# Optimization experiments

Measured on AMD Instinct MI355X. Metric: run time of the kernel, lower is better.

## Reference

```python
import jax, jax.numpy as jnp
import numpy as np

B, S, DIM = 2, 2048, 4096
N_HEADS, N_KV_HEADS = 32, 8
HEAD_DIM = DIM // N_HEADS  # 128
N_REP = N_HEADS // N_KV_HEADS  # 4
NEG_INF = -1e9


def setup_inputs() -> dict:
    key = jax.random.key(0)
    ks = jax.random.split(key, 6)
    x = jax.random.normal(ks[0], (B, S, DIM), dtype=jnp.float32)
    # torch Linear weights are [out_features, in_features]
    sc = 0.02
    wq = jax.random.normal(ks[1], (N_HEADS * HEAD_DIM, DIM), dtype=jnp.float32) * sc
    wk = jax.random.normal(ks[2], (N_KV_HEADS * HEAD_DIM, DIM), dtype=jnp.float32) * sc
    wv = jax.random.normal(ks[3], (N_KV_HEADS * HEAD_DIM, DIM), dtype=jnp.float32) * sc
    wo = jax.random.normal(ks[4], (DIM, N_HEADS * HEAD_DIM), dtype=jnp.float32) * sc
    # RoPE frequencies, matching llama precompute_freqs_cis (theta=10000)
    inv = 1.0 / (10000.0 ** (np.arange(0, HEAD_DIM, 2, dtype=np.float32) / HEAD_DIM))
    t = np.arange(S, dtype=np.float32)
    freqs = np.outer(t, inv)  # [S, HEAD_DIM//2]
    freqs_cos = jnp.asarray(np.cos(freqs), dtype=jnp.float32)
    freqs_sin = jnp.asarray(np.sin(freqs), dtype=jnp.float32)
    # causal mask: 0 on/below diagonal, large negative above
    mask = jnp.triu(jnp.full((S, S), NEG_INF, dtype=jnp.float32), k=1)
    return {"x": x, "wq": wq, "wk": wk, "wv": wv, "wo": wo,
            "freqs_cos": freqs_cos, "freqs_sin": freqs_sin,
            "mask": mask, "start_pos": 0}


def _apply_rope(t, cos, sin):
    # t: [b, s, h, hd]; complex mult on interleaved (even, odd) pairs
    tr, ti = t[..., 0::2], t[..., 1::2]
    cos = cos[None, :, None, :]
    sin = sin[None, :, None, :]
    out_r = tr * cos - ti * sin
    out_i = tr * sin + ti * cos
    return jnp.stack([out_r, out_i], axis=-1).reshape(t.shape)


def reference(x, wq, wk, wv, wo, freqs_cos, freqs_sin, mask, start_pos):
    bsz, seqlen, _ = x.shape
    xq = (x @ wq.T).reshape(bsz, seqlen, N_HEADS, HEAD_DIM)
    xk = (x @ wk.T).reshape(bsz, seqlen, N_KV_HEADS, HEAD_DIM)
    xv = (x @ wv.T).reshape(bsz, seqlen, N_KV_HEADS, HEAD_DIM)
    xq = _apply_rope(xq, freqs_cos, freqs_sin)
    xk = _apply_rope(xk, freqs_cos, freqs_sin)
    # prefill: start_pos == 0, so cache slice == current keys/values
    # GQA repeat_kv via broadcast (torch repeat_interleave over head dim)
    keys = jnp.broadcast_to(xk[:, :, :, None, :],
                            (bsz, seqlen, N_KV_HEADS, N_REP, HEAD_DIM)
                            ).reshape(bsz, seqlen, N_HEADS, HEAD_DIM)
    values = jnp.broadcast_to(xv[:, :, :, None, :],
                              (bsz, seqlen, N_KV_HEADS, N_REP, HEAD_DIM)
                              ).reshape(bsz, seqlen, N_HEADS, HEAD_DIM)
    scale = 1.0 / jnp.sqrt(jnp.float32(HEAD_DIM))
    # [b, h, q, k]
    scores = jnp.einsum('bqhd,bkhd->bhqk', xq, keys) * scale
    scores = scores + mask[None, None, :, :]
    probs = jax.nn.softmax(scores.astype(jnp.float32), axis=-1).astype(xq.dtype)
    out = jnp.einsum('bhqk,bkhd->bqhd', probs, values)
    out = out.reshape(bsz, seqlen, N_HEADS * HEAD_DIM)
    return out @ wo.T
```

## Files before the change

### kernel.cpp

```cpp
#include <hip/hip_runtime.h>

typedef unsigned short u16;
typedef unsigned int u32;
typedef __bf16 bf16_t;
typedef bf16_t bf16x8 __attribute__((ext_vector_type(8)));
typedef float f32x4 __attribute__((ext_vector_type(4)));

#define B_ 2
#define S_ 2048
#define DIM_ 4096
#define NH_ 32
#define NKV_ 8
#define HD_ 128

__device__ __forceinline__ u16 f2b(float f) {
  union { float f; unsigned u; } x; x.f = f;
  unsigned r = x.u + 0x7fffu + ((x.u >> 16) & 1u);
  return (u16)(r >> 16);
}
__device__ __forceinline__ float b2f(u16 u) {
  union { unsigned u; float f; } x; x.u = ((unsigned)u) << 16;
  return x.f;
}
__device__ __forceinline__ u32 cvtpk(float lo, float hi) {
  u32 r;
  asm volatile("v_cvt_pk_bf16_f32 %0, %1, %2" : "=v"(r) : "v"(lo), "v"(hi));
  return r;
}

#define GLDS(gsrc, ldst) \
  __builtin_amdgcn_global_load_lds((const __attribute__((address_space(1))) void*)(gsrc), \
                                   (__attribute__((address_space(3))) void*)(ldst), 16, 0, 0)
#define BAR()    __builtin_amdgcn_s_barrier()
#define SCHED0() __builtin_amdgcn_sched_barrier(0)

__global__ void cvt_kernel(const float* __restrict__ in, u16* __restrict__ out, int n4) {
  int i = blockIdx.x * blockDim.x + threadIdx.x;
  int stride = gridDim.x * blockDim.x;
  for (; i < n4; i += stride) {
    float4 v = ((const float4*)in)[i];
    ushort4 o;
    o.x = f2b(v.x); o.y = f2b(v.y); o.z = f2b(v.z); o.w = f2b(v.w);
    ((ushort4*)out)[i] = o;
  }
}

__global__ void rope_kernel(u16* __restrict__ t, const float* __restrict__ fc,
                            const float* __restrict__ fs, int nheads) {
  int idx = blockIdx.x * blockDim.x + threadIdx.x;
  int ppr = nheads * 64;
  int row = idx / ppr;
  int pr = idx - row * ppr;
  int h = pr >> 6, j = pr & 63;
  int s = row & (S_ - 1);
  float c = fc[s * 64 + j], sn = fs[s * 64 + j];
  u16* p = t + (size_t)row * (size_t)(nheads * HD_) + h * HD_ + j * 2;
  float tr = b2f(p[0]), ti = b2f(p[1]);
  p[0] = f2b(tr * c - ti * sn);
  p[1] = f2b(tr * sn + ti * c);
}

template<int MODE>
__global__ __launch_bounds__(512, 2) void gemm256(const u16* __restrict__ A,
                                                  const u16* __restrict__ B,
                                                  void* __restrict__ Cout,
                                                  void* __restrict__ Cout2,
                                                  int M, int N, int K) {
  __shared__ u16 As[2][2][128 * 64];
  __shared__ u16 Bs[2][2][128 * 64];
  const int nbn = N >> 8;
  const int nwg = gridDim.x;
  int wg = blockIdx.x;
  wg = (wg & 7) * (nwg >> 3) + (wg >> 3);
  const int bm = wg / nbn;
  const int bn = wg - bm * nbn;
  const int tid = threadIdx.x;
  const int lane = tid & 63;
  const int wv = tid >> 6;
  const int wm = wv >> 2, wn = wv & 3;
  const int qloc = lane & 15, grp = lane >> 4;
  const int NT = K >> 6;

  f32x4 acc[8][4];
#pragma unroll
  for (int i = 0; i < 8; i++)
#pragma unroll
    for (int j = 0; j < 4; j++)
#pragma unroll
      for (int r = 0; r < 4; r++) acc[i][j][r] = 0.0f;

  const int srowl = lane >> 3;
  const int scsw = 8 * ((lane & 7) ^ srowl);
  const size_t rowA = (size_t)(bm * 256 + wv * 16 + srowl) * K + scsw;
  const size_t rowB = (size_t)(bn * 256 + wv * 16 + srowl) * K + scsw;

#define STAGE_A(buf, h, tt) { \
    GLDS(A + rowA + (size_t)((h) * 128) * K + (size_t)(tt) * 64, &As[buf][h][wv * 1024]); \
    GLDS(A + rowA + (size_t)((h) * 128 + 8) * K + (size_t)(tt) * 64, &As[buf][h][wv * 1024 + 512]); }
#define STAGE_B(buf, h, tt) { \
    GLDS(B + rowB + (size_t)((h) * 128) * K + (size_t)(tt) * 64, &Bs[buf][h][wv * 1024]); \
    GLDS(B + rowB + (size_t)((h) * 128 + 8) * K + (size_t)(tt) * 64, &Bs[buf][h][wv * 1024 + 512]); }

  STAGE_A(0, 0, 0); STAGE_A(0, 1, 0);
  STAGE_B(0, 0, 0); STAGE_B(0, 1, 0);
  STAGE_B(1, 0, 1); STAGE_B(1, 1, 1);
  asm volatile("s_waitcnt vmcnt(4)" ::: "memory");
  BAR();

  for (int t = 0; t < NT; t += 2) {
#pragma unroll
    for (int half = 0; half < 2; half++) {
      bf16x8 bfr[4][2];
#pragma unroll
      for (int qd = 0; qd < 4; qd++) {
        if (qd == 0) {
#pragma unroll
          for (int j = 0; j < 4; j++)
#pragma unroll
            for (int ks = 0; ks < 2; ks++) {
              int rb = (wn & 1) * 64 + j * 16 + qloc;
              bfr[j][ks] = *(const bf16x8*)((const char*)&Bs[half][wn >> 1][0]
                           + rb * 128 + ((ks * 64 + grp * 16) ^ ((rb & 7) << 4)));
            }
        }
        bf16x8 af[2][2];
#pragma unroll
        for (int ii = 0; ii < 2; ii++)
#pragma unroll
          for (int ks = 0; ks < 2; ks++) {
            int rh = qd * 32 + ii * 16 + qloc;
            af[ii][ks] = *(const bf16x8*)((const char*)&As[half][wm][0]
                         + rh * 128 + ((ks * 64 + grp * 16) ^ ((rh & 7) << 4)));
          }
        const int ph = half * 4 + qd;
        if (ph == 0)      { STAGE_A(1, 0, t + 1); }
        else if (ph == 1) { STAGE_A(1, 1, t + 1); }
        else if (ph == 2) { if (t + 2 < NT) STAGE_B(0, 0, t + 2); }
        else if (ph == 3) { if (t + 2 < NT) STAGE_B(0, 1, t + 2); }
        else if (ph == 4) { if (t + 2 < NT) STAGE_A(0, 0, t + 2); }
        else if (ph == 5) { if (t + 2 < NT) STAGE_A(0, 1, t + 2); }
        else if (ph == 6) { if (t + 3 < NT) STAGE_B(1, 0, t + 3); }
        else              { if (t + 3 < NT) STAGE_B(1, 1, t + 3); }
        BAR();
        __builtin_amdgcn_s_setprio(1);
#pragma unroll
        for (int ii = 0; ii < 2; ii++)
#pragma unroll
          for (int ks = 0; ks < 2; ks++)
#pragma unroll
            for (int j = 0; j < 4; j++)
              acc[qd * 2 + ii][j] = __builtin_amdgcn_mfma_f32_16x16x32_bf16(
                  af[ii][ks], bfr[j][ks], acc[qd * 2 + ii][j], 0, 0, 0);
        __builtin_amdgcn_s_setprio(0);
        SCHED0();
        if (qd == 3) {
          if ((half == 0 ? t + 2 : t + 3) < NT)
            asm volatile("s_waitcnt vmcnt(4)" ::: "memory");
          else
            asm volatile("s_waitcnt vmcnt(0)" ::: "memory");
        }
        BAR();
      }
    }
  }
#undef STAGE_A
#undef STAGE_B

  const int r0g = bm * 256 + wm * 128 + grp * 4;
  const int c0g = bn * 256 + wn * 64 + qloc;
#pragma unroll
  for (int i = 0; i < 8; i++)
#pragma unroll
    for (int j = 0; j < 4; j++)
#pragma unroll
      for (int r = 0; r < 4; r++) {
        int row = r0g + i * 16 + r;
        int col = c0g + j * 16;
        float v = acc[i][j][r];
        if (MODE == 1)      ((float*)Cout)[(size_t)row * N + col] = v;
        else if (MODE == 0) ((u16*)Cout)[(size_t)row * N + col]  = f2b(v);
        else {
          if (col < 1024) ((u16*)Cout)[(size_t)row * 1024 + col] = f2b(v);
          else            ((u16*)Cout2)[(size_t)(col - 1024) * M + row] = f2b(v);
        }
      }
}

__global__ __launch_bounds__(256) void attn_kernel(const u16* __restrict__ Q,
                                                   const u16* __restrict__ Kt,
                                                   const u16* __restrict__ VT,
                                                   u16* __restrict__ O) {
  __shared__ u16 Ks[2][32 * 128];
  __shared__ u16 Vs[2][32 * 128];
  __shared__ u16 Ps[4][16 * 40];

  const int bid = blockIdx.x;
  const int qb = 31 - (bid >> 6);
  const int h = bid & 31;
  const int b = (bid >> 5) & 1;
  const int g = h >> 2;
  const int tid = threadIdx.x;
  const int lane = tid & 63;
  const int wv = tid >> 6;
  const int qrow0 = qb * 64 + wv * 16;
  const float scale = 0.08838834764831845f;

  bf16x8 qf[4];
  {
    const int qr = qrow0 + (lane & 15);
    const u16* qptr = Q + (size_t)(b * S_ + qr) * (NH_ * HD_) + h * HD_ + (lane >> 4) * 8;
#pragma unroll
    for (int c = 0; c < 4; c++) qf[c] = *(const bf16x8*)(qptr + c * 32);
  }

  float m = -1e30f, l = 0.f;
  f32x4 o[8];
#pragma unroll
  for (int c = 0; c < 8; c++)
#pragma unroll
    for (int r = 0; r < 4; r++) o[c][r] = 0.f;

  const int nkv = 2 * qb + 2;

  const int kkey_ = wv * 4 + (lane >> 4);
  const int kcb_ = (lane & 15) * 16;
  const int vd_ = wv * 16 + (lane >> 2);
  const int vkb_ = (lane & 3) * 16;

  auto STAGE = [&](int t, int buf) {
#pragma unroll
    for (int p = 0; p < 2; p++) {
      int key = p * 16 + kkey_;
      int cbs = kcb_ ^ ((key & 7) << 4);
      const u16* ksrc = Kt + (size_t)(b * S_ + t * 32 + key) * (NKV_ * HD_) + g * HD_ + (cbs >> 1);
      GLDS(ksrc, &Ks[buf][(p * 4 + wv) * 512]);
      int d = p * 64 + vd_;
      int kbs = vkb_ ^ (((d >> 1) & 3) << 4);
      const u16* vsrc = VT + (size_t)(g * HD_ + d) * (B_ * S_) + b * S_ + t * 32 + (kbs >> 1);
      GLDS(vsrc, &Vs[buf][(p * 4 + wv) * 512]);
    }
  };

  STAGE(0, 0);
  int cur = 0;

  const int qloc = lane & 15;
  const int grp = lane >> 4;
  u16* psrow = &Ps[wv][qloc * 40];

  for (int t = 0; t < nkv; t++) {
    const bool pf = (t + 1 < nkv);
    if (pf) {
      STAGE(t + 1, cur ^ 1);
      asm volatile("s_waitcnt vmcnt(4)" ::: "memory");
    } else {
      asm volatile("s_waitcnt vmcnt(0)" ::: "memory");
    }
    BAR();
    SCHED0();

    if (t * 32 <= qrow0 + 15) {
      f32x4 s[2];
      __builtin_amdgcn_s_setprio(1);
#pragma unroll
      for (int n = 0; n < 2; n++) {
        f32x4 sc;
#pragma unroll
        for (int r = 0; r < 4; r++) sc[r] = 0.f;
        int krow = n * 16 + qloc;
#pragma unroll
        for (int c = 0; c < 4; c++) {
          int colb = c * 64 + (grp * 16);
          int addr = krow * 256 + (colb ^ ((krow & 7) << 4));
          bf16x8 kf = *(const bf16x8*)((const char*)Ks[cur] + addr);
          sc = __builtin_amdgcn_mfma_f32_16x16x32_bf16(kf, qf[c], sc, 0, 0, 0);
        }
        s[n] = sc;
      }
      __builtin_amdgcn_s_setprio(0);
      const int q = qrow0 + qloc;
      if (t * 32 + 31 > qrow0) {
#pragma unroll
        for (int n = 0; n < 2; n++)
#pragma unroll
          for (int r = 0; r < 4; r++) {
            int k = t * 32 + n * 16 + grp * 4 + r;
            if (k > q) s[n][r] = -1e9f;
          }
      }
      float pmax = fmaxf(fmaxf(fmaxf(s[0][0], s[0][1]), fmaxf(s[0][2], s[0][3])),
                         fmaxf(fmaxf(s[1][0], s[1][1]), fmaxf(s[1][2], s[1][3])));
      pmax = fmaxf(pmax, __shfl_xor(pmax, 16));
      pmax = fmaxf(pmax, __shfl_xor(pmax, 32));
      if (__any(pmax > m + 64.f)) {
        float mn = fmaxf(m, pmax);
        float alpha = __expf(scale * (m - mn));
        m = mn;
        l *= alpha;
        float ar[4];
#pragma unroll
        for (int r = 0; r < 4; r++) ar[r] = __shfl(alpha, grp * 4 + r);
#pragma unroll
        for (int c = 0; c < 8; c++)
#pragma unroll
          for (int r = 0; r < 4; r++) o[c][r] *= ar[r];
      }
      const float msc = m * scale;
      float p[2][4];
#pragma unroll
      for (int n = 0; n < 2; n++)
#pragma unroll
        for (int r = 0; r < 4; r++)
          p[n][r] = __expf(fmaf(s[n][r], scale, -msc));
      float rs = ((p[0][0] + p[0][1]) + (p[0][2] + p[0][3])) +
                 ((p[1][0] + p[1][1]) + (p[1][2] + p[1][3]));
      rs += __shfl_xor(rs, 16);
      rs += __shfl_xor(rs, 32);
      l += rs;
      {
        u32 w[2][2];
#pragma unroll
        for (int n = 0; n < 2; n++) {
          w[n][0] = cvtpk(p[n][0], p[n][1]);
          w[n][1] = cvtpk(p[n][2], p[n][3]);
        }
        *(u32*)&psrow[0 * 16 + grp * 4]     = w[0][0];
        *(u32*)&psrow[0 * 16 + grp * 4 + 2] = w[0][1];
        *(u32*)&psrow[1 * 16 + grp * 4]     = w[1][0];
        *(u32*)&psrow[1 * 16 + grp * 4 + 2] = w[1][1];
      }
      asm volatile("s_waitcnt lgkmcnt(0)" ::: "memory");
      SCHED0();
      bf16x8 pa = *(const bf16x8*)&psrow[grp * 8];
      __builtin_amdgcn_s_setprio(1);
#pragma unroll
      for (int c = 0; c < 8; c++) {
        int d = c * 16 + qloc;
        int addr = d * 64 + ((grp * 16) ^ (((d >> 1) & 3) << 4));
        bf16x8 vf = *(const bf16x8*)((const char*)Vs[cur] + addr);
        o[c] = __builtin_amdgcn_mfma_f32_16x16x32_bf16(pa, vf, o[c], 0, 0, 0);
      }
      __builtin_amdgcn_s_setprio(0);
    }
    asm volatile("s_waitcnt lgkmcnt(0)" ::: "memory");
    SCHED0();
    BAR();
    cur ^= 1;
  }

  float lr[4];
#pragma unroll
  for (int r = 0; r < 4; r++) lr[r] = 1.0f / __shfl(l, grp * 4 + r);
#pragma unroll
  for (int c = 0; c < 8; c++)
#pragma unroll
    for (int r = 0; r < 4; r++) {
      int qo = qrow0 + grp * 4 + r;
      float val = o[c][r] * lr[r];
      O[(size_t)(b * S_ + qo) * (NH_ * HD_) + h * HD_ + c * 16 + qloc] = f2b(val);
    }
}

extern "C" void kernel_launch(void* const* d_in, const int* in_sizes, int n_in,
                              void* d_out, int out_size, void* d_ws, size_t ws_size,
                              hipStream_t stream) {
  const float* x  = (const float*)d_in[0];
  const float* wq = (const float*)d_in[1];
  const float* wk = (const float*)d_in[2];
  const float* wv = (const float*)d_in[3];
  const float* wo = (const float*)d_in[4];
  const float* fc = (const float*)d_in[5];
  const float* fs = (const float*)d_in[6];

  char* ws = (char*)d_ws;
  u16* Xb  = (u16*)(ws);
  u16* Wqb = (u16*)(ws + 33554432);
  u16* Wkv = (u16*)(ws + 67108864);
  u16* Qw  = (u16*)(ws + 83886080);
  u16* Kw  = (u16*)(ws + 117440512);
  u16* Vw  = (u16*)(ws + 125829120);
  u16* Ow  = Xb;
  u16* Wob = Wqb;

  auto cvt = [&](const float* in, u16* out, int n) {
    int n4 = n >> 2;
    int blocks = (n4 + 255) / 256; if (blocks > 2048) blocks = 2048;
    cvt_kernel<<<dim3(blocks), dim3(256), 0, stream>>>(in, out, n4);
  };
  cvt(x,  Xb,  B_ * S_ * DIM_);
  cvt(wq, Wqb, DIM_ * DIM_);
  cvt(wk, Wkv, NKV_ * HD_ * DIM_);
  cvt(wv, Wkv + (size_t)1024 * 4096, NKV_ * HD_ * DIM_);

  gemm256<0><<<dim3(16 * 16), 512, 0, stream>>>(Xb, Wqb, Qw, nullptr, 4096, 4096, 4096);
  gemm256<3><<<dim3(16 * 8),  512, 0, stream>>>(Xb, Wkv, Kw, Vw, 4096, 2048, 4096);

  cvt(wo, Wob, DIM_ * DIM_);

  rope_kernel<<<dim3((B_ * S_ * NH_ * 64) / 256), 256, 0, stream>>>(Qw, fc, fs, NH_);
  rope_kernel<<<dim3((B_ * S_ * NKV_ * 64) / 256), 256, 0, stream>>>(Kw, fc, fs, NKV_);

  attn_kernel<<<dim3(B_ * NH_ * (S_ / 64)), 256, 0, stream>>>(Qw, Kw, Vw, Ow);

  gemm256<1><<<dim3(16 * 16), 512, 0, stream>>>(Ow, Wob, d_out, nullptr, 4096, 4096, 4096);
}
```

Before: 578.2 us.

## Double attention query tile per block and fuse Q RoPE into attention

Each wave now processes 32 query rows (two 16-row fragments) instead of 16, so each block covers 128 queries and every staged K/V tile is reused for twice as many MFMAs, halving K/V global traffic and barrier count per query. The separate RoPE pass over Q is removed and applied while loading Q fragments in the attention kernel, which saves one full read and write of the Q tensor. In exchange the kernel uses more registers (double the accumulators) and launches half as many blocks, which lowers occupancy and coarsens causal load balance.

```diff
diff --git a/kernel.cpp b/kernel.cpp
--- a/kernel.cpp
+++ b/kernel.cpp
@@ -189,41 +189,64 @@
 __global__ __launch_bounds__(256) void attn_kernel(const u16* __restrict__ Q,
                                                    const u16* __restrict__ Kt,
                                                    const u16* __restrict__ VT,
-                                                   u16* __restrict__ O) {
+                                                   u16* __restrict__ O,
+                                                   const float* __restrict__ fc,
+                                                   const float* __restrict__ fs) {
   __shared__ u16 Ks[2][32 * 128];
   __shared__ u16 Vs[2][32 * 128];
-  __shared__ u16 Ps[4][16 * 40];
+  __shared__ u16 Ps[4][32 * 40];
 
   const int bid = blockIdx.x;
-  const int qb = 31 - (bid >> 6);
+  const int qb = 15 - (bid >> 6);
   const int h = bid & 31;
   const int b = (bid >> 5) & 1;
   const int g = h >> 2;
   const int tid = threadIdx.x;
   const int lane = tid & 63;
   const int wv = tid >> 6;
-  const int qrow0 = qb * 64 + wv * 16;
+  const int qrow0 = qb * 128 + wv * 32;
   const float scale = 0.08838834764831845f;
 
-  bf16x8 qf[4];
-  {
-    const int qr = qrow0 + (lane & 15);
-    const u16* qptr = Q + (size_t)(b * S_ + qr) * (NH_ * HD_) + h * HD_ + (lane >> 4) * 8;
-#pragma unroll
-    for (int c = 0; c < 4; c++) qf[c] = *(const bf16x8*)(qptr + c * 32);
+  const int qloc = lane & 15;
+  const int grp = lane >> 4;
+
+  bf16x8 qf[2][4];
+#pragma unroll
+  for (int f = 0; f < 2; f++) {
+    const int qr = qrow0 + f * 16 + qloc;
+    const u16* qptr = Q + (size_t)(b * S_ + qr) * (NH_ * HD_) + h * HD_ + grp * 8;
+#pragma unroll
+    for (int c = 0; c < 4; c++) {
+      union { bf16x8 v; u16 u[8]; } raw;
+      raw.v = *(const bf16x8*)(qptr + c * 32);
+      const int p0 = c * 16 + grp * 4;
+      const float4 cv = *(const float4*)&fc[(size_t)qr * 64 + p0];
+      const float4 sv = *(const float4*)&fs[(size_t)qr * 64 + p0];
+      union { bf16x8 v; u32 w[4]; } out;
+      const float cc[4] = {cv.x, cv.y, cv.z, cv.w};
+      const float ss[4] = {sv.x, sv.y, sv.z, sv.w};
+#pragma unroll
+      for (int j = 0; j < 4; j++) {
+        float tr = b2f(raw.u[2 * j]), ti = b2f(raw.u[2 * j + 1]);
+        out.w[j] = cvtpk(tr * cc[j] - ti * ss[j], tr * ss[j] + ti * cc[j]);
+      }
+      qf[f][c] = out.v;
+    }
   }
 
-  float m = -1e30f, l = 0.f;
-  f32x4 o[8];
-#pragma unroll
-  for (int c = 0; c < 8; c++)
-#pragma unroll
-    for (int r = 0; r < 4; r++) o[c][r] = 0.f;
-
-  const int nkv = 2 * qb + 2;
-
-  const int kkey_ = wv * 4 + (lane >> 4);
-  const int kcb_ = (lane & 15) * 16;
+  float m[2] = {-1e30f, -1e30f}, l[2] = {0.f, 0.f};
+  f32x4 o[2][8];
+#pragma unroll
+  for (int f = 0; f < 2; f++)
+#pragma unroll
+    for (int c = 0; c < 8; c++)
+#pragma unroll
+      for (int r = 0; r < 4; r++) o[f][c][r] = 0.f;
+
+  const int nkv = 4 * qb + 4;
+
+  const int kkey_ = wv * 4 + grp;
+  const int kcb_ = qloc * 16;
   const int vd_ = wv * 16 + (lane >> 2);
   const int vkb_ = (lane & 3) * 16;
 
@@ -244,9 +267,7 @@
   STAGE(0, 0);
   int cur = 0;
 
-  const int qloc = lane & 15;
-  const int grp = lane >> 4;
-  u16* psrow = &Ps[wv][qloc * 40];
+  u16* psbase = &Ps[wv][0];
 
   for (int t = 0; t < nkv; t++) {
     const bool pf = (t + 1 < nkv);
@@ -259,86 +280,99 @@
     BAR();
     SCHED0();
 
-    if (t * 32 <= qrow0 + 15) {
-      f32x4 s[2];
+    if (t * 32 <= qrow0 + 31) {
+      f32x4 s[2][2];
+#pragma unroll
+      for (int f = 0; f < 2; f++)
+#pragma unroll
+        for (int n = 0; n < 2; n++)
+#pragma unroll
+          for (int r = 0; r < 4; r++) s[f][n][r] = 0.f;
       __builtin_amdgcn_s_setprio(1);
 #pragma unroll
       for (int n = 0; n < 2; n++) {
-        f32x4 sc;
-#pragma unroll
-        for (int r = 0; r < 4; r++) sc[r] = 0.f;
         int krow = n * 16 + qloc;
 #pragma unroll
         for (int c = 0; c < 4; c++) {
           int colb = c * 64 + (grp * 16);
           int addr = krow * 256 + (colb ^ ((krow & 7) << 4));
           bf16x8 kf = *(const bf16x8*)((const char*)Ks[cur] + addr);
-          sc = __builtin_amdgcn_mfma_f32_16x16x32_bf16(kf, qf[c], sc, 0, 0, 0);
-        }
-        s[n] = sc;
+          s[0][n] = __builtin_amdgcn_mfma_f32_16x16x32_bf16(kf, qf[0][c], s[0][n], 0, 0, 0);
+          s[1][n] = __builtin_amdgcn_mfma_f32_16x16x32_bf16(kf, qf[1][c], s[1][n], 0, 0, 0);
+        }
       }
       __builtin_amdgcn_s_setprio(0);
-      const int q = qrow0 + qloc;
       if (t * 32 + 31 > qrow0) {
 #pragma unroll
+        for (int f = 0; f < 2; f++) {
+          const int q = qrow0 + f * 16 + qloc;
+#pragma unroll
+          for (int n = 0; n < 2; n++)
+#pragma unroll
+            for (int r = 0; r < 4; r++) {
+              int k = t * 32 + n * 16 + grp * 4 + r;
+              if (k > q) s[f][n][r] = -1e9f;
+            }
+        }
+      }
+      float pmax[2];
+#pragma unroll
+      for (int f = 0; f < 2; f++) {
+        pmax[f] = fmaxf(fmaxf(fmaxf(s[f][0][0], s[f][0][1]), fmaxf(s[f][0][2], s[f][0][3])),
+                        fmaxf(fmaxf(s[f][1][0], s[f][1][1]), fmaxf(s[f][1][2], s[f][1][3])));
+        pmax[f] = fmaxf(pmax[f], __shfl_xor(pmax[f], 16));
+        pmax[f] = fmaxf(pmax[f], __shfl_xor(pmax[f], 32));
+      }
+      bool need = (pmax[0] > m[0] + 64.f) || (pmax[1] > m[1] + 64.f);
+      if (__any(need)) {
+#pragma unroll
+        for (int f = 0; f < 2; f++) {
+          float mn = fmaxf(m[f], pmax[f]);
+          float alpha = __expf(scale * (m[f] - mn));
+          m[f] = mn;
+          l[f] *= alpha;
+          float ar[4];
+#pragma unroll
+          for (int r = 0; r < 4; r++) ar[r] = __shfl(alpha, grp * 4 + r);
+#pragma unroll
+          for (int c = 0; c < 8; c++)
+#pragma unroll
+            for (int r = 0; r < 4; r++) o[f][c][r] *= ar[r];
+        }
+      }
+#pragma unroll
+      for (int f = 0; f < 2; f++) {
+        const float msc = m[f] * scale;
+        float p[2][4];
+#pragma unroll
         for (int n = 0; n < 2; n++)
 #pragma unroll
-          for (int r = 0; r < 4; r++) {
-            int k = t * 32 + n * 16 + grp * 4 + r;
-            if (k > q) s[n][r] = -1e9f;
-          }
-      }
-      float pmax = fmaxf(fmaxf(fmaxf(s[0][0], s[0][1]), fmaxf(s[0][2], s[0][3])),
-                         fmaxf(fmaxf(s[1][0], s[1][1]), fmaxf(s[1][2], s[1][3])));
-      pmax = fmaxf(pmax, __shfl_xor(pmax, 16));
-      pmax = fmaxf(pmax, __shfl_xor(pmax, 32));
-      if (__any(pmax > m + 64.f)) {
-        float mn = fmaxf(m, pmax);
-        float alpha = __expf(scale * (m - mn));
-        m = mn;
-        l *= alpha;
-        float ar[4];
-#pragma unroll
-        for (int r = 0; r < 4; r++) ar[r] = __shfl(alpha, grp * 4 + r);
-#pragma unroll
-        for (int c = 0; c < 8; c++)
-#pragma unroll
-          for (int r = 0; r < 4; r++) o[c][r] *= ar[r];
-      }
-      const float msc = m * scale;
-      float p[2][4];
-#pragma unroll
-      for (int n = 0; n < 2; n++)
-#pragma unroll
-        for (int r = 0; r < 4; r++)
-          p[n][r] = __expf(fmaf(s[n][r], scale, -msc));
-      float rs = ((p[0][0] + p[0][1]) + (p[0][2] + p[0][3])) +
-                 ((p[1][0] + p[1][1]) + (p[1][2] + p[1][3]));
-      rs += __shfl_xor(rs, 16);
-      rs += __shfl_xor(rs, 32);
-      l += rs;
-      {
-        u32 w[2][2];
-#pragma unroll
-        for (int n = 0; n < 2; n++) {
-          w[n][0] = cvtpk(p[n][0], p[n][1]);
-          w[n][1] = cvtpk(p[n][2], p[n][3]);
-        }
-        *(u32*)&psrow[0 * 16 + grp * 4]     = w[0][0];
-        *(u32*)&psrow[0 * 16 + grp * 4 + 2] = w[0][1];
-        *(u32*)&psrow[1 * 16 + grp * 4]     = w[1][0];
-        *(u32*)&psrow[1 * 16 + grp * 4 + 2] = w[1][1];
+          for (int r = 0; r < 4; r++)
+            p[n][r] = __expf(fmaf(s[f][n][r], scale, -msc));
+        float rs = ((p[0][0] + p[0][1]) + (p[0][2] + p[0][3])) +
+                   ((p[1][0] + p[1][1]) + (p[1][2] + p[1][3]));
+        rs += __shfl_xor(rs, 16);
+        rs += __shfl_xor(rs, 32);
+        l[f] += rs;
+        u16* psrow = psbase + (f * 16 + qloc) * 40;
+        *(u32*)&psrow[0 * 16 + grp * 4]     = cvtpk(p[0][0], p[0][1]);
+        *(u32*)&psrow[0 * 16 + grp * 4 + 2] = cvtpk(p[0][2], p[0][3]);
+        *(u32*)&psrow[1 * 16 + grp * 4]     = cvtpk(p[1][0], p[1][1]);
+        *(u32*)&psrow[1 * 16 + grp * 4 + 2] = cvtpk(p[1][2], p[1][3]);
       }
       asm volatile("s_waitcnt lgkmcnt(0)" ::: "memory");
       SCHED0();
-      bf16x8 pa = *(const bf16x8*)&psrow[grp * 8];
+      bf16x8 pa[2];
+      pa[0] = *(const bf16x8*)&psbase[(0 * 16 + qloc) * 40 + grp * 8];
+      pa[1] = *(const bf16x8*)&psbase[(1 * 16 + qloc) * 40 + grp * 8];
       __builtin_amdgcn_s_setprio(1);
 #pragma unroll
       for (int c = 0; c < 8; c++) {
         int d = c * 16 + qloc;
         int addr = d * 64 + ((grp * 16) ^ (((d >> 1) & 3) << 4));
         bf16x8 vf = *(const bf16x8*)((const char*)Vs[cur] + addr);
-        o[c] = __builtin_amdgcn_mfma_f32_16x16x32_bf16(pa, vf, o[c], 0, 0, 0);
+        o[0][c] = __builtin_amdgcn_mfma_f32_16x16x32_bf16(pa[0], vf, o[0][c], 0, 0, 0);
+        o[1][c] = __builtin_amdgcn_mfma_f32_16x16x32_bf16(pa[1], vf, o[1][c], 0, 0, 0);
       }
       __builtin_amdgcn_s_setprio(0);
     }
@@ -348,17 +382,20 @@
     cur ^= 1;
   }
 
-  float lr[4];
-#pragma unroll
-  for (int r = 0; r < 4; r++) lr[r] = 1.0f / __shfl(l, grp * 4 + r);
-#pragma unroll
-  for (int c = 0; c < 8; c++)
-#pragma unroll
-    for (int r = 0; r < 4; r++) {
-      int qo = qrow0 + grp * 4 + r;
-      float val = o[c][r] * lr[r];
-      O[(size_t)(b * S_ + qo) * (NH_ * HD_) + h * HD_ + c * 16 + qloc] = f2b(val);
-    }
+#pragma unroll
+  for (int f = 0; f < 2; f++) {
+    float lr[4];
+#pragma unroll
+    for (int r = 0; r < 4; r++) lr[r] = 1.0f / __shfl(l[f], grp * 4 + r);
+#pragma unroll
+    for (int c = 0; c < 8; c++)
+#pragma unroll
+      for (int r = 0; r < 4; r++) {
+        int qo = qrow0 + f * 16 + grp * 4 + r;
+        float val = o[f][c][r] * lr[r];
+        O[(size_t)(b * S_ + qo) * (NH_ * HD_) + h * HD_ + c * 16 + qloc] = f2b(val);
+      }
+  }
 }
 
 extern "C" void kernel_launch(void* const* d_in, const int* in_sizes, int n_in,
@@ -397,10 +434,9 @@
 
   cvt(wo, Wob, DIM_ * DIM_);
 
-  rope_kernel<<<dim3((B_ * S_ * NH_ * 64) / 256), 256, 0, stream>>>(Qw, fc, fs, NH_);
   rope_kernel<<<dim3((B_ * S_ * NKV_ * 64) / 256), 256, 0, stream>>>(Kw, fc, fs, NKV_);
 
-  attn_kernel<<<dim3(B_ * NH_ * (S_ / 64)), 256, 0, stream>>>(Qw, Kw, Vw, Ow);
+  attn_kernel<<<dim3(B_ * NH_ * (S_ / 128)), 256, 0, stream>>>(Qw, Kw, Vw, Ow, fc, fs);
 
   gemm256<1><<<dim3(16 * 16), 512, 0, stream>>>(Ow, Wob, d_out, nullptr, 4096, 4096, 4096);
 }
```

Result: faster. 566.3 us (-2.1%).

## Fuse QKV GEMMs, fold Q RoPE into attention, use permlane for P

Applied to the files above, without the earlier changes.

Concatenates Wq, Wk and Wv into one weight buffer so a single 384-workgroup GEMM writes Q, K and transposed V, replacing two GEMM launches. Q rotary embedding is applied inside the attention kernel when the Q fragments are loaded, which removes one rope kernel pass over Q. The P matrix is rearranged with v_permlane32/16 swaps instead of a round trip through LDS, and softmax uses exp2 with a pre-scaled log2e constant. This removes launches, memory traffic and LDS syncs, but the permlane lane mapping must match the MFMA A-operand layout.

```diff
diff --git a/kernel.cpp b/kernel.cpp
--- a/kernel.cpp
+++ b/kernel.cpp
@@ -65,6 +65,7 @@
                                                   const u16* __restrict__ B,
                                                   void* __restrict__ Cout,
                                                   void* __restrict__ Cout2,
+                                                  void* __restrict__ Cout3,
                                                   int M, int N, int K) {
   __shared__ u16 As[2][2][128 * 64];
   __shared__ u16 Bs[2][2][128 * 64];
@@ -177,11 +178,11 @@
         int row = r0g + i * 16 + r;
         int col = c0g + j * 16;
         float v = acc[i][j][r];
-        if (MODE == 1)      ((float*)Cout)[(size_t)row * N + col] = v;
-        else if (MODE == 0) ((u16*)Cout)[(size_t)row * N + col]  = f2b(v);
+        if (MODE == 1) ((float*)Cout)[(size_t)row * N + col] = v;
         else {
-          if (col < 1024) ((u16*)Cout)[(size_t)row * 1024 + col] = f2b(v);
-          else            ((u16*)Cout2)[(size_t)(col - 1024) * M + row] = f2b(v);
+          if (col < 4096)      ((u16*)Cout)[(size_t)row * 4096 + col] = f2b(v);
+          else if (col < 5120) ((u16*)Cout2)[(size_t)row * 1024 + (col - 4096)] = f2b(v);
+          else                 ((u16*)Cout3)[(size_t)(col - 5120) * M + row] = f2b(v);
         }
       }
 }
@@ -189,10 +190,11 @@
 __global__ __launch_bounds__(256) void attn_kernel(const u16* __restrict__ Q,
                                                    const u16* __restrict__ Kt,
                                                    const u16* __restrict__ VT,
-                                                   u16* __restrict__ O) {
+                                                   u16* __restrict__ O,
+                                                   const float* __restrict__ fc,
+                                                   const float* __restrict__ fs) {
   __shared__ u16 Ks[2][32 * 128];
   __shared__ u16 Vs[2][32 * 128];
-  __shared__ u16 Ps[4][16 * 40];
 
   const int bid = blockIdx.x;
   const int qb = 31 - (bid >> 6);
@@ -203,14 +205,32 @@
   const int lane = tid & 63;
   const int wv = tid >> 6;
   const int qrow0 = qb * 64 + wv * 16;
-  const float scale = 0.08838834764831845f;
+  const float scl2 = 0.12751744f;
+
+  const int qloc = lane & 15;
+  const int grp = lane >> 4;
 
   bf16x8 qf[4];
   {
-    const int qr = qrow0 + (lane & 15);
-    const u16* qptr = Q + (size_t)(b * S_ + qr) * (NH_ * HD_) + h * HD_ + (lane >> 4) * 8;
-#pragma unroll
-    for (int c = 0; c < 4; c++) qf[c] = *(const bf16x8*)(qptr + c * 32);
+    const int qr = qrow0 + qloc;
+    const u16* qptr = Q + (size_t)(b * S_ + qr) * (NH_ * HD_) + h * HD_ + grp * 8;
+#pragma unroll
+    for (int c = 0; c < 4; c++) {
+      union { bf16x8 v; u16 u[8]; } raw;
+      raw.v = *(const bf16x8*)(qptr + c * 32);
+      const int p0 = c * 16 + grp * 4;
+      const float4 cv = *(const float4*)&fc[(size_t)qr * 64 + p0];
+      const float4 sv = *(const float4*)&fs[(size_t)qr * 64 + p0];
+      union { bf16x8 v; u32 w[4]; } out;
+      const float cc[4] = {cv.x, cv.y, cv.z, cv.w};
+      const float ss[4] = {sv.x, sv.y, sv.z, sv.w};
+#pragma unroll
+      for (int j = 0; j < 4; j++) {
+        float tr = b2f(raw.u[2 * j]), ti = b2f(raw.u[2 * j + 1]);
+        out.w[j] = cvtpk(tr * cc[j] - ti * ss[j], tr * ss[j] + ti * cc[j]);
+      }
+      qf[c] = out.v;
+    }
   }
 
   float m = -1e30f, l = 0.f;
@@ -222,8 +242,8 @@
 
   const int nkv = 2 * qb + 2;
 
-  const int kkey_ = wv * 4 + (lane >> 4);
-  const int kcb_ = (lane & 15) * 16;
+  const int kkey_ = wv * 4 + grp;
+  const int kcb_ = qloc * 16;
   const int vd_ = wv * 16 + (lane >> 2);
   const int vkb_ = (lane & 3) * 16;
 
@@ -244,10 +264,6 @@
   STAGE(0, 0);
   int cur = 0;
 
-  const int qloc = lane & 15;
-  const int grp = lane >> 4;
-  u16* psrow = &Ps[wv][qloc * 40];
-
   for (int t = 0; t < nkv; t++) {
     const bool pf = (t + 1 < nkv);
     if (pf) {
@@ -294,7 +310,7 @@
       pmax = fmaxf(pmax, __shfl_xor(pmax, 32));
       if (__any(pmax > m + 64.f)) {
         float mn = fmaxf(m, pmax);
-        float alpha = __expf(scale * (m - mn));
+        float alpha = exp2f((m - mn) * scl2);
         m = mn;
         l *= alpha;
         float ar[4];
@@ -305,33 +321,29 @@
 #pragma unroll
           for (int r = 0; r < 4; r++) o[c][r] *= ar[r];
       }
-      const float msc = m * scale;
+      const float msc = m * scl2;
       float p[2][4];
 #pragma unroll
       for (int n = 0; n < 2; n++)
 #pragma unroll
         for (int r = 0; r < 4; r++)
-          p[n][r] = __expf(fmaf(s[n][r], scale, -msc));
+          p[n][r] = exp2f(fmaf(s[n][r], scl2, -msc));
       float rs = ((p[0][0] + p[0][1]) + (p[0][2] + p[0][3])) +
                  ((p[1][0] + p[1][1]) + (p[1][2] + p[1][3]));
       rs += __shfl_xor(rs, 16);
       rs += __shfl_xor(rs, 32);
       l += rs;
-      {
-        u32 w[2][2];
-#pragma unroll
-        for (int n = 0; n < 2; n++) {
-          w[n][0] = cvtpk(p[n][0], p[n][1]);
-          w[n][1] = cvtpk(p[n][2], p[n][3]);
-        }
-        *(u32*)&psrow[0 * 16 + grp * 4]     = w[0][0];
-        *(u32*)&psrow[0 * 16 + grp * 4 + 2] = w[0][1];
-        *(u32*)&psrow[1 * 16 + grp * 4]     = w[1][0];
-        *(u32*)&psrow[1 * 16 + grp * 4 + 2] = w[1][1];
-      }
-      asm volatile("s_waitcnt lgkmcnt(0)" ::: "memory");
-      SCHED0();
-      bf16x8 pa = *(const bf16x8*)&psrow[grp * 8];
+      u32 a0 = cvtpk(p[0][0], p[0][1]);
+      u32 a1 = cvtpk(p[0][2], p[0][3]);
+      u32 b0 = cvtpk(p[1][0], p[1][1]);
+      u32 b1 = cvtpk(p[1][2], p[1][3]);
+      asm volatile("v_permlane32_swap_b32 %0, %1" : "+v"(a0), "+v"(b0));
+      asm volatile("v_permlane32_swap_b32 %0, %1" : "+v"(a1), "+v"(b1));
+      asm volatile("v_permlane16_swap_b32 %0, %1" : "+v"(a0), "+v"(b0));
+      asm volatile("v_permlane16_swap_b32 %0, %1" : "+v"(a1), "+v"(b1));
+      union { bf16x8 v; u32 w[4]; } pau;
+      pau.w[0] = a0; pau.w[1] = a1; pau.w[2] = b0; pau.w[3] = b1;
+      bf16x8 pa = pau.v;
       __builtin_amdgcn_s_setprio(1);
 #pragma unroll
       for (int c = 0; c < 8; c++) {
@@ -373,14 +385,13 @@
   const float* fs = (const float*)d_in[6];
 
   char* ws = (char*)d_ws;
-  u16* Xb  = (u16*)(ws);
-  u16* Wqb = (u16*)(ws + 33554432);
-  u16* Wkv = (u16*)(ws + 67108864);
-  u16* Qw  = (u16*)(ws + 83886080);
-  u16* Kw  = (u16*)(ws + 117440512);
-  u16* Vw  = (u16*)(ws + 125829120);
-  u16* Ow  = Xb;
-  u16* Wob = Wqb;
+  u16* Xb   = (u16*)(ws);
+  u16* Wqkv = (u16*)(ws + 33554432);
+  u16* Qw   = (u16*)(ws + 83886080);
+  u16* Kw   = (u16*)(ws + 117440512);
+  u16* Vw   = (u16*)(ws + 125829120);
+  u16* Ow   = Xb;
+  u16* Wob  = Wqkv;
 
   auto cvt = [&](const float* in, u16* out, int n) {
     int n4 = n >> 2;
@@ -388,19 +399,17 @@
     cvt_kernel<<<dim3(blocks), dim3(256), 0, stream>>>(in, out, n4);
   };
   cvt(x,  Xb,  B_ * S_ * DIM_);
-  cvt(wq, Wqb, DIM_ * DIM_);
-  cvt(wk, Wkv, NKV_ * HD_ * DIM_);
-  cvt(wv, Wkv + (size_t)1024 * 4096, NKV_ * HD_ * DIM_);
-
-  gemm256<0><<<dim3(16 * 16), 512, 0, stream>>>(Xb, Wqb, Qw, nullptr, 4096, 4096, 4096);
-  gemm256<3><<<dim3(16 * 8),  512, 0, stream>>>(Xb, Wkv, Kw, Vw, 4096, 2048, 4096);
+  cvt(wq, Wqkv, DIM_ * DIM_);
+  cvt(wk, Wqkv + (size_t)4096 * 4096, NKV_ * HD_ * DIM_);
+  cvt(wv, Wqkv + (size_t)5120 * 4096, NKV_ * HD_ * DIM_);
+
+  gemm256<4><<<dim3(16 * 24), 512, 0, stream>>>(Xb, Wqkv, Qw, Kw, Vw, 4096, 6144, 4096);
 
   cvt(wo, Wob, DIM_ * DIM_);
 
-  rope_kernel<<<dim3((B_ * S_ * NH_ * 64) / 256), 256, 0, stream>>>(Qw, fc, fs, NH_);
   rope_kernel<<<dim3((B_ * S_ * NKV_ * 64) / 256), 256, 0, stream>>>(Kw, fc, fs, NKV_);
 
-  attn_kernel<<<dim3(B_ * NH_ * (S_ / 64)), 256, 0, stream>>>(Qw, Kw, Vw, Ow);
-
-  gemm256<1><<<dim3(16 * 16), 512, 0, stream>>>(Ow, Wob, d_out, nullptr, 4096, 4096, 4096);
-}
+  attn_kernel<<<dim3(B_ * NH_ * (S_ / 64)), 256, 0, stream>>>(Qw, Kw, Vw, Ow, fc, fs);
+
+  gemm256<1><<<dim3(16 * 16), 512, 0, stream>>>(Ow, Wob, d_out, nullptr, nullptr, 4096, 4096, 4096);
+}
```

Result: no change. 568.0 us (-1.8%).
